# Kernel optimization log

Hardware: AMD Instinct MI355X
Metric: run time of the kernel (lower is better)

## Reference

```python
import jax, jax.numpy as jnp
import numpy as np

B, N, C = 1, 4096, 1024
H = 16
HD = C // H  # head_dim = 64
SCALE = HD ** -0.5


def setup_inputs() -> dict:
    key = jax.random.key(0)
    k1, k2, k3, k4, k5 = jax.random.split(key, 5)
    x1 = jax.random.normal(k1, (B, N, C), dtype=jnp.float32)
    x2 = jax.random.normal(k2, (B, N, C), dtype=jnp.float32)
    # qkv: Linear(dim, 2*all_head_dim), bias=False. Stored as (in, out) for x @ W.
    W_qkv = jax.random.normal(k3, (C, 2 * H * HD), dtype=jnp.float32) * (C ** -0.5)
    # proj: Linear(all_head_dim, dim) with bias
    W_proj = jax.random.normal(k4, (H * HD, C), dtype=jnp.float32) * ((H * HD) ** -0.5)
    b_proj = jax.random.normal(k5, (C,), dtype=jnp.float32) * 0.01
    return {"x1": x1, "x2": x2, "W_qkv": W_qkv, "W_proj": W_proj, "b_proj": b_proj}


def reference(x1, x2, W_qkv, W_proj, b_proj):
    b, n, c = x1.shape
    # qk projection: (B,N,2*H*HD) -> (2,B,H,N,HD)
    qkv = (x1 @ W_qkv).reshape(b, n, 2, H, HD).transpose(2, 0, 3, 1, 4)
    q, k = qkv[0], qkv[1]  # (B,H,N,HD)
    # V2: reshape (N,1,H,HD) then permute -> (1,H,N,HD); valid since B==1
    v = x2.reshape(n, 1, H, HD).transpose(1, 2, 0, 3)
    attn = jax.nn.softmax(jnp.einsum('bhnd,bhmd->bhnm', q * SCALE, k), axis=-1)
    out = jnp.einsum('bhnm,bhmd->bhnd', attn, v)  # broadcasts v over batch
    out = out.transpose(0, 2, 1, 3).reshape(b, n, H * HD)
    return out @ W_proj + b_proj
```

## Files before the change

kernel.cpp:

```cpp
#include <hip/hip_runtime.h>

typedef unsigned short u16;
typedef unsigned int u32;

#define HNUM 16
#define NSEQ 4096
#define CDIM 1024
#define SCALE 0.125f
#define LOG2E 1.4426950408889634f

using bf16x8 = __attribute__((ext_vector_type(8))) __bf16;
using f32x4  = __attribute__((ext_vector_type(4))) float;

__device__ __forceinline__ u16 f2bf(float f) {
  union { float f; u32 u; } v; v.f = f;
  u32 u = v.u;
  return (u16)((u + 0x7fffu + ((u >> 16) & 1u)) >> 16);
}
__device__ __forceinline__ float fexp2(float x) { return __builtin_amdgcn_exp2f(x); }

__device__ __forceinline__ f32x4 mfma16(bf16x8 a, bf16x8 b, f32x4 c) {
  return __builtin_amdgcn_mfma_f32_16x16x32_bf16(a, b, c, 0, 0, 0);
}

__device__ __forceinline__ u32 pack2(float a, float b) {
  union { float f; u32 u; } A, B;
  A.f = a; B.f = b;
  return __builtin_amdgcn_perm(B.u + 0x8000u, A.u + 0x8000u, 0x07060302u);
}

__device__ __forceinline__ void g2l16(const void* g, void* l) {
  __builtin_amdgcn_global_load_lds(
      (const __attribute__((address_space(1))) unsigned int*)(unsigned long long)g,
      (__attribute__((address_space(3))) unsigned int*)(unsigned int)(unsigned long long)l,
      16, 0, 0);
}

__global__ __launch_bounds__(256) void cvt_k(const float* __restrict__ in,
                                             u16* __restrict__ out) {
  const int i = (blockIdx.x * 256 + threadIdx.x) * 8;
  const float4 f0 = *(const float4*)(in + i);
  const float4 f1 = *(const float4*)(in + i + 4);
  u32 d[4] = {pack2(f0.x, f0.y), pack2(f0.z, f0.w),
              pack2(f1.x, f1.y), pack2(f1.z, f1.w)};
  *(bf16x8*)(out + i) = *(bf16x8*)d;
}

__global__ __launch_bounds__(256) void cvtT_k(const float* __restrict__ in,
                                              u16* __restrict__ out, int R, int C,
                                              int scaleRows, float scale) {
  __shared__ u16 t[64][65];
  const int tid = threadIdx.x;
  const int r0 = blockIdx.y * 64, c0 = blockIdx.x * 64;
  const int tr = tid >> 2, tc = (tid & 3) * 16;
  const float s = (c0 < scaleRows) ? scale : 1.0f;
  const float* src = in + (r0 + tr) * C + c0 + tc;
#pragma unroll
  for (int i = 0; i < 16; ++i) t[tr][tc + i] = f2bf(src[i] * s);
  __syncthreads();
  u16* dst = out + (c0 + tr) * R + r0 + tc;
#pragma unroll
  for (int i = 0; i < 16; ++i) dst[i] = t[tc + i][tr];
}

__global__ __launch_bounds__(256) void gemm1_k(const u16* __restrict__ A,
                                               const u16* __restrict__ Bt,
                                               u16* __restrict__ C,
                                               int M, int N, int K) {
  __shared__ __align__(16) u16 As[128 * 64];
  __shared__ __align__(16) u16 Bs[128 * 64];
  const int tid = threadIdx.x;
  const int wave = tid >> 6, lane = tid & 63;
  const int quad = lane >> 4, l16 = lane & 15;
  const int m0 = blockIdx.y * 128, n0 = blockIdx.x * 128;
  const int wm = (wave >> 1) * 64, wn = (wave & 1) * 64;
  const int lrow = lane >> 3, lc8 = (lane & 7) * 8;

  f32x4 acc[4][4] = {};
  for (int k0 = 0; k0 < K; k0 += 64) {
#pragma unroll
    for (int c = 0; c < 4; ++c) {
      const int cw = wave * 4 + c;
      g2l16(A  + (m0 + cw * 8 + lrow) * K + k0 + lc8, (char*)As + cw * 1024);
      g2l16(Bt + (n0 + cw * 8 + lrow) * K + k0 + lc8, (char*)Bs + cw * 1024);
    }
    __syncthreads();
#pragma unroll
    for (int ks = 0; ks < 2; ++ks) {
      bf16x8 a[4], b[4];
#pragma unroll
      for (int mt = 0; mt < 4; ++mt)
        a[mt] = *(const bf16x8*)(As + (wm + mt * 16 + l16) * 64 + ks * 32 + quad * 8);
#pragma unroll
      for (int nt = 0; nt < 4; ++nt)
        b[nt] = *(const bf16x8*)(Bs + (wn + nt * 16 + l16) * 64 + ks * 32 + quad * 8);
#pragma unroll
      for (int mt = 0; mt < 4; ++mt)
#pragma unroll
        for (int nt = 0; nt < 4; ++nt)
          acc[mt][nt] = mfma16(a[mt], b[nt], acc[mt][nt]);
    }
    __syncthreads();
  }
#pragma unroll
  for (int mt = 0; mt < 4; ++mt)
#pragma unroll
    for (int nt = 0; nt < 4; ++nt)
#pragma unroll
      for (int r = 0; r < 4; ++r)
        C[(m0 + wm + mt * 16 + quad * 4 + r) * N + n0 + wn + nt * 16 + l16] =
            f2bf(acc[mt][nt][r]);
}

__global__ __launch_bounds__(256) void gemm2_k(const u16* __restrict__ A,
                                               const u16* __restrict__ Bt,
                                               float* __restrict__ C,
                                               const float* __restrict__ bias,
                                               int M, int N, int K) {
  __shared__ __align__(16) u16 As[128 * 64];
  __shared__ __align__(16) u16 Bs[64 * 64];
  const int tid = threadIdx.x;
  const int wave = tid >> 6, lane = tid & 63;
  const int quad = lane >> 4, l16 = lane & 15;
  const int m0 = blockIdx.y * 128, n0 = blockIdx.x * 64;
  const int wm = wave * 32;
  const int lrow = lane >> 3, lc8 = (lane & 7) * 8;

  f32x4 acc[2][4] = {};
  for (int k0 = 0; k0 < K; k0 += 64) {
#pragma unroll
    for (int c = 0; c < 4; ++c) {
      const int cw = wave * 4 + c;
      g2l16(A + (m0 + cw * 8 + lrow) * K + k0 + lc8, (char*)As + cw * 1024);
    }
#pragma unroll
    for (int c = 0; c < 2; ++c) {
      const int cw = wave * 2 + c;
      g2l16(Bt + (n0 + cw * 8 + lrow) * K + k0 + lc8, (char*)Bs + cw * 1024);
    }
    __syncthreads();
#pragma unroll
    for (int ks = 0; ks < 2; ++ks) {
      bf16x8 a[2], b[4];
#pragma unroll
      for (int mt = 0; mt < 2; ++mt)
        a[mt] = *(const bf16x8*)(As + (wm + mt * 16 + l16) * 64 + ks * 32 + quad * 8);
#pragma unroll
      for (int nt = 0; nt < 4; ++nt)
        b[nt] = *(const bf16x8*)(Bs + (nt * 16 + l16) * 64 + ks * 32 + quad * 8);
#pragma unroll
      for (int mt = 0; mt < 2; ++mt)
#pragma unroll
        for (int nt = 0; nt < 4; ++nt)
          acc[mt][nt] = mfma16(a[mt], b[nt], acc[mt][nt]);
    }
    __syncthreads();
  }
#pragma unroll
  for (int mt = 0; mt < 2; ++mt)
#pragma unroll
    for (int nt = 0; nt < 4; ++nt)
#pragma unroll
      for (int r = 0; r < 4; ++r) {
        const int col = n0 + nt * 16 + l16;
        C[(m0 + wm + mt * 16 + quad * 4 + r) * N + col] = acc[mt][nt][r] + bias[col];
      }
}

__global__ __launch_bounds__(128) void attn_k(const u16* __restrict__ QK,
                                              const u16* __restrict__ Vt,
                                              u16* __restrict__ O) {
  __shared__ __align__(16) u16 Ks[2][64 * 64];
  __shared__ __align__(16) u16 Vs[2][64 * 64];
  __shared__ __align__(16) u16 Ps[2][32 * 64];
  const int tid = threadIdx.x;
  const int wave = tid >> 6, lane = tid & 63;
  const int quad = lane >> 4, l16 = lane & 15;
  const int head = blockIdx.y;
  const int qb = blockIdx.x * 64 + wave * 32;
  const int lrow = lane >> 3;
  const int lc8 = ((lane & 7) ^ lrow) * 8;
  const int swz = (quad ^ (l16 & 7)) * 8;

  const u16* kp[4];
  const u16* vp[4];
#pragma unroll
  for (int c = 0; c < 4; ++c) {
    const int row = (wave * 4 + c) * 8 + lrow;
    kp[c] = QK + row * 2048 + CDIM + head * 64 + lc8;
    vp[c] = Vt + (head * 64 + row) * NSEQ + lc8;
  }

  bf16x8 qf[2][2];
#pragma unroll
  for (int mt = 0; mt < 2; ++mt)
#pragma unroll
    for (int ks = 0; ks < 2; ++ks)
      qf[mt][ks] = *(const bf16x8*)(QK + (qb + mt * 16 + l16) * 2048 + head * 64 +
                                    ks * 32 + quad * 8);

  f32x4 o[2][4] = {};
  float lsum[2] = {};
  bf16x8 pfr[2][2];
  bf16x8 vfr[2][4];
  u16* Pw = Ps[wave];

#pragma unroll
  for (int c = 0; c < 4; ++c) {
    const int cw = wave * 4 + c;
    g2l16(kp[c], (char*)Ks[0] + cw * 1024);
    g2l16(vp[c], (char*)Vs[0] + cw * 1024);
    kp[c] += 64 * 2048;
    vp[c] += 64;
  }

  for (int kt = 0; kt < NSEQ / 64; ++kt) {
    const int cur = kt & 1;
    __syncthreads();

    if (kt > 0) {
#pragma unroll
      for (int ks = 0; ks < 2; ++ks)
#pragma unroll
        for (int dt = 0; dt < 4; ++dt)
#pragma unroll
          for (int mt = 0; mt < 2; ++mt)
            o[mt][dt] = mfma16(pfr[mt][ks], vfr[ks][dt], o[mt][dt]);
    }

    if (kt < NSEQ / 64 - 1) {
#pragma unroll
      for (int c = 0; c < 4; ++c) {
        const int cw = wave * 4 + c;
        g2l16(kp[c], (char*)Ks[1 - cur] + cw * 1024);
        g2l16(vp[c], (char*)Vs[1 - cur] + cw * 1024);
        kp[c] += 64 * 2048;
        vp[c] += 64;
      }
    }

    const u16* Kc = Ks[cur];
    const u16* Vc = Vs[cur];

    f32x4 s[2][4] = {};
#pragma unroll
    for (int ks = 0; ks < 2; ++ks)
#pragma unroll
      for (int nt = 0; nt < 4; ++nt) {
        const bf16x8 kf =
            *(const bf16x8*)(Kc + (nt * 16 + l16) * 64 + (swz ^ (ks * 32)));
#pragma unroll
        for (int mt = 0; mt < 2; ++mt)
          s[mt][nt] = mfma16(kf, qf[mt][ks], s[mt][nt]);
      }

#pragma unroll
    for (int mt = 0; mt < 2; ++mt)
#pragma unroll
      for (int nt = 0; nt < 4; ++nt) {
        const float p0 = fexp2(s[mt][nt][0]);
        const float p1 = fexp2(s[mt][nt][1]);
        const float p2 = fexp2(s[mt][nt][2]);
        const float p3 = fexp2(s[mt][nt][3]);
        lsum[mt] += (p0 + p1) + (p2 + p3);
        u32 d01 = pack2(p0, p1), d23 = pack2(p2, p3);
        const int col8 = (nt * 2 + (quad >> 1)) ^ (l16 & 7);
        u32* dst = (u32*)(Pw + (mt * 16 + l16) * 64 + col8 * 8 + (quad & 1) * 4);
        dst[0] = d01; dst[1] = d23;
      }

#pragma unroll
    for (int mt = 0; mt < 2; ++mt)
#pragma unroll
      for (int ks = 0; ks < 2; ++ks)
        pfr[mt][ks] = *(const bf16x8*)(Pw + (mt * 16 + l16) * 64 + (swz ^ (ks * 32)));
#pragma unroll
    for (int ks = 0; ks < 2; ++ks)
#pragma unroll
      for (int dt = 0; dt < 4; ++dt)
        vfr[ks][dt] =
            *(const bf16x8*)(Vc + (dt * 16 + l16) * 64 + (swz ^ (ks * 32)));
  }

#pragma unroll
  for (int ks = 0; ks < 2; ++ks)
#pragma unroll
    for (int dt = 0; dt < 4; ++dt)
#pragma unroll
      for (int mt = 0; mt < 2; ++mt)
        o[mt][dt] = mfma16(pfr[mt][ks], vfr[ks][dt], o[mt][dt]);

  float linv[2];
#pragma unroll
  for (int mt = 0; mt < 2; ++mt) {
    float v = lsum[mt];
    v += __shfl_xor(v, 16, 64);
    v += __shfl_xor(v, 32, 64);
    linv[mt] = 1.0f / v;
  }
#pragma unroll
  for (int mt = 0; mt < 2; ++mt)
#pragma unroll
    for (int r = 0; r < 4; ++r) {
      const float lv = __shfl(linv[mt], (lane & 48) | (quad * 4 + r), 64);
#pragma unroll
      for (int dt = 0; dt < 4; ++dt)
        O[(qb + mt * 16 + quad * 4 + r) * CDIM + head * 64 + dt * 16 + l16] =
            f2bf(o[mt][dt][r] * lv);
    }
}

extern "C" void kernel_launch(void* const* d_in, const int* in_sizes, int n_in,
                              void* d_out, int out_size, void* d_ws, size_t ws_size,
                              hipStream_t stream) {
  const float* x1    = (const float*)d_in[0];
  const float* x2    = (const float*)d_in[1];
  const float* Wqkv  = (const float*)d_in[2];
  const float* Wproj = (const float*)d_in[3];
  const float* bproj = (const float*)d_in[4];
  float* out = (float*)d_out;

  char* ws = (char*)d_ws;
  u16* QK  = (u16*)(ws);
  u16* Vt  = (u16*)(ws + 16u * 1024 * 1024);
  u16* Obf = (u16*)(ws + 24u * 1024 * 1024);
  u16* WpT = (u16*)(ws + 32u * 1024 * 1024);
  u16* WqT = (u16*)(ws + 34u * 1024 * 1024);
  u16* x1b = (u16*)(ws + 38u * 1024 * 1024);

  const float cfac = SCALE * LOG2E;

  cvt_k<<<dim3(4096 * 1024 / 2048), 256, 0, stream>>>(x1, x1b);
  cvtT_k<<<dim3(2048 / 64, 1024 / 64), 256, 0, stream>>>(Wqkv, WqT, 1024, 2048,
                                                         1024, cfac);
  cvtT_k<<<dim3(1024 / 64, 1024 / 64), 256, 0, stream>>>(Wproj, WpT, 1024, 1024,
                                                         0, 1.0f);
  cvtT_k<<<dim3(1024 / 64, 4096 / 64), 256, 0, stream>>>(x2, Vt, 4096, 1024,
                                                         0, 1.0f);

  gemm1_k<<<dim3(2048 / 128, 4096 / 128), 256, 0, stream>>>(x1b, WqT, QK,
                                                            4096, 2048, 1024);
  attn_k<<<dim3(4096 / 64, HNUM), 128, 0, stream>>>(QK, Vt, Obf);
  gemm2_k<<<dim3(1024 / 64, 4096 / 128), 256, 0, stream>>>(Obf, WpT, out, bproj,
                                                           4096, 1024, 1024);
}
```

Before: 249.6 us.

## Double-buffer GEMM LDS tiles and load attention K/V straight to registers

Both projection GEMMs gain a second LDS buffer. The next K-slice is prefetched while the current one feeds MFMAs, which removes one barrier per iteration. The attention kernel drops its shared K/V staging entirely: each wave loads K and V fragments from global memory into registers, prefetching the next K tile while the softmax runs, and keeps only the per-wave P buffer in LDS. This removes block-wide barriers and LDS traffic in attention, but each wave now fetches K/V separately with strided 16-byte loads, which relies on L2 and adds register pressure.

```diff
diff --git a/kernel.cpp b/kernel.cpp
--- a/kernel.cpp
+++ b/kernel.cpp
@@ -67,8 +67,8 @@
                                                const u16* __restrict__ Bt,
                                                u16* __restrict__ C,
                                                int M, int N, int K) {
-  __shared__ __align__(16) u16 As[128 * 64];
-  __shared__ __align__(16) u16 Bs[128 * 64];
+  __shared__ __align__(16) u16 As[2][128 * 64];
+  __shared__ __align__(16) u16 Bs[2][128 * 64];
   const int tid = threadIdx.x;
   const int wave = tid >> 6, lane = tid & 63;
   const int quad = lane >> 4, l16 = lane & 15;
@@ -77,30 +77,40 @@
   const int lrow = lane >> 3, lc8 = (lane & 7) * 8;
 
   f32x4 acc[4][4] = {};
-  for (int k0 = 0; k0 < K; k0 += 64) {
-#pragma unroll
-    for (int c = 0; c < 4; ++c) {
-      const int cw = wave * 4 + c;
-      g2l16(A  + (m0 + cw * 8 + lrow) * K + k0 + lc8, (char*)As + cw * 1024);
-      g2l16(Bt + (n0 + cw * 8 + lrow) * K + k0 + lc8, (char*)Bs + cw * 1024);
-    }
+#pragma unroll
+  for (int c = 0; c < 4; ++c) {
+    const int cw = wave * 4 + c;
+    g2l16(A  + (m0 + cw * 8 + lrow) * K + lc8, (char*)As[0] + cw * 1024);
+    g2l16(Bt + (n0 + cw * 8 + lrow) * K + lc8, (char*)Bs[0] + cw * 1024);
+  }
+  const int NIT = K / 64;
+  for (int it = 0; it < NIT; ++it) {
+    const int cur = it & 1;
     __syncthreads();
+    if (it + 1 < NIT) {
+      const int k0 = (it + 1) * 64;
+#pragma unroll
+      for (int c = 0; c < 4; ++c) {
+        const int cw = wave * 4 + c;
+        g2l16(A  + (m0 + cw * 8 + lrow) * K + k0 + lc8, (char*)As[1 - cur] + cw * 1024);
+        g2l16(Bt + (n0 + cw * 8 + lrow) * K + k0 + lc8, (char*)Bs[1 - cur] + cw * 1024);
+      }
+    }
 #pragma unroll
     for (int ks = 0; ks < 2; ++ks) {
       bf16x8 a[4], b[4];
 #pragma unroll
       for (int mt = 0; mt < 4; ++mt)
-        a[mt] = *(const bf16x8*)(As + (wm + mt * 16 + l16) * 64 + ks * 32 + quad * 8);
+        a[mt] = *(const bf16x8*)(As[cur] + (wm + mt * 16 + l16) * 64 + ks * 32 + quad * 8);
 #pragma unroll
       for (int nt = 0; nt < 4; ++nt)
-        b[nt] = *(const bf16x8*)(Bs + (wn + nt * 16 + l16) * 64 + ks * 32 + quad * 8);
+        b[nt] = *(const bf16x8*)(Bs[cur] + (wn + nt * 16 + l16) * 64 + ks * 32 + quad * 8);
 #pragma unroll
       for (int mt = 0; mt < 4; ++mt)
 #pragma unroll
         for (int nt = 0; nt < 4; ++nt)
           acc[mt][nt] = mfma16(a[mt], b[nt], acc[mt][nt]);
     }
-    __syncthreads();
   }
 #pragma unroll
   for (int mt = 0; mt < 4; ++mt)
@@ -117,8 +127,8 @@
                                                float* __restrict__ C,
                                                const float* __restrict__ bias,
                                                int M, int N, int K) {
-  __shared__ __align__(16) u16 As[128 * 64];
-  __shared__ __align__(16) u16 Bs[64 * 64];
+  __shared__ __align__(16) u16 As[2][128 * 64];
+  __shared__ __align__(16) u16 Bs[2][64 * 64];
   const int tid = threadIdx.x;
   const int wave = tid >> 6, lane = tid & 63;
   const int quad = lane >> 4, l16 = lane & 15;
@@ -127,34 +137,48 @@
   const int lrow = lane >> 3, lc8 = (lane & 7) * 8;
 
   f32x4 acc[2][4] = {};
-  for (int k0 = 0; k0 < K; k0 += 64) {
-#pragma unroll
-    for (int c = 0; c < 4; ++c) {
-      const int cw = wave * 4 + c;
-      g2l16(A + (m0 + cw * 8 + lrow) * K + k0 + lc8, (char*)As + cw * 1024);
-    }
-#pragma unroll
-    for (int c = 0; c < 2; ++c) {
-      const int cw = wave * 2 + c;
-      g2l16(Bt + (n0 + cw * 8 + lrow) * K + k0 + lc8, (char*)Bs + cw * 1024);
-    }
+#pragma unroll
+  for (int c = 0; c < 4; ++c) {
+    const int cw = wave * 4 + c;
+    g2l16(A + (m0 + cw * 8 + lrow) * K + lc8, (char*)As[0] + cw * 1024);
+  }
+#pragma unroll
+  for (int c = 0; c < 2; ++c) {
+    const int cw = wave * 2 + c;
+    g2l16(Bt + (n0 + cw * 8 + lrow) * K + lc8, (char*)Bs[0] + cw * 1024);
+  }
+  const int NIT = K / 64;
+  for (int it = 0; it < NIT; ++it) {
+    const int cur = it & 1;
     __syncthreads();
+    if (it + 1 < NIT) {
+      const int k0 = (it + 1) * 64;
+#pragma unroll
+      for (int c = 0; c < 4; ++c) {
+        const int cw = wave * 4 + c;
+        g2l16(A + (m0 + cw * 8 + lrow) * K + k0 + lc8, (char*)As[1 - cur] + cw * 1024);
+      }
+#pragma unroll
+      for (int c = 0; c < 2; ++c) {
+        const int cw = wave * 2 + c;
+        g2l16(Bt + (n0 + cw * 8 + lrow) * K + k0 + lc8, (char*)Bs[1 - cur] + cw * 1024);
+      }
+    }
 #pragma unroll
     for (int ks = 0; ks < 2; ++ks) {
       bf16x8 a[2], b[4];
 #pragma unroll
       for (int mt = 0; mt < 2; ++mt)
-        a[mt] = *(const bf16x8*)(As + (wm + mt * 16 + l16) * 64 + ks * 32 + quad * 8);
+        a[mt] = *(const bf16x8*)(As[cur] + (wm + mt * 16 + l16) * 64 + ks * 32 + quad * 8);
 #pragma unroll
       for (int nt = 0; nt < 4; ++nt)
-        b[nt] = *(const bf16x8*)(Bs + (nt * 16 + l16) * 64 + ks * 32 + quad * 8);
+        b[nt] = *(const bf16x8*)(Bs[cur] + (nt * 16 + l16) * 64 + ks * 32 + quad * 8);
 #pragma unroll
       for (int mt = 0; mt < 2; ++mt)
 #pragma unroll
         for (int nt = 0; nt < 4; ++nt)
           acc[mt][nt] = mfma16(a[mt], b[nt], acc[mt][nt]);
     }
-    __syncthreads();
   }
 #pragma unroll
   for (int mt = 0; mt < 2; ++mt)
@@ -170,26 +194,16 @@
 __global__ __launch_bounds__(128) void attn_k(const u16* __restrict__ QK,
                                               const u16* __restrict__ Vt,
                                               u16* __restrict__ O) {
-  __shared__ __align__(16) u16 Ks[2][64 * 64];
-  __shared__ __align__(16) u16 Vs[2][64 * 64];
   __shared__ __align__(16) u16 Ps[2][32 * 64];
   const int tid = threadIdx.x;
   const int wave = tid >> 6, lane = tid & 63;
   const int quad = lane >> 4, l16 = lane & 15;
   const int head = blockIdx.y;
   const int qb = blockIdx.x * 64 + wave * 32;
-  const int lrow = lane >> 3;
-  const int lc8 = ((lane & 7) ^ lrow) * 8;
   const int swz = (quad ^ (l16 & 7)) * 8;
 
-  const u16* kp[4];
-  const u16* vp[4];
-#pragma unroll
-  for (int c = 0; c < 4; ++c) {
-    const int row = (wave * 4 + c) * 8 + lrow;
-    kp[c] = QK + row * 2048 + CDIM + head * 64 + lc8;
-    vp[c] = Vt + (head * 64 + row) * NSEQ + lc8;
-  }
+  const u16* kbase = QK + l16 * 2048 + CDIM + head * 64 + quad * 8;
+  const u16* vbase = Vt + (head * 64 + l16) * 4096 + quad * 8;
 
   bf16x8 qf[2][2];
 #pragma unroll
@@ -201,58 +215,40 @@
 
   f32x4 o[2][4] = {};
   float lsum[2] = {};
-  bf16x8 pfr[2][2];
-  bf16x8 vfr[2][4];
   u16* Pw = Ps[wave];
 
-#pragma unroll
-  for (int c = 0; c < 4; ++c) {
-    const int cw = wave * 4 + c;
-    g2l16(kp[c], (char*)Ks[0] + cw * 1024);
-    g2l16(vp[c], (char*)Vs[0] + cw * 1024);
-    kp[c] += 64 * 2048;
-    vp[c] += 64;
-  }
-
-  for (int kt = 0; kt < NSEQ / 64; ++kt) {
-    const int cur = kt & 1;
-    __syncthreads();
-
-    if (kt > 0) {
+  bf16x8 kf[2][4];
+#pragma unroll
+  for (int ks = 0; ks < 2; ++ks)
+#pragma unroll
+    for (int nt = 0; nt < 4; ++nt)
+      kf[ks][nt] = *(const bf16x8*)(kbase + (nt * 16) * 2048 + ks * 32);
+
+  for (int kt0 = 0; kt0 < NSEQ; kt0 += 64) {
+    bf16x8 vf[2][4];
+#pragma unroll
+    for (int ks = 0; ks < 2; ++ks)
+#pragma unroll
+      for (int dt = 0; dt < 4; ++dt)
+        vf[ks][dt] = *(const bf16x8*)(vbase + (dt * 16) * 4096 + kt0 + ks * 32);
+
+    f32x4 s[2][4] = {};
+#pragma unroll
+    for (int ks = 0; ks < 2; ++ks)
+#pragma unroll
+      for (int nt = 0; nt < 4; ++nt)
+#pragma unroll
+        for (int mt = 0; mt < 2; ++mt)
+          s[mt][nt] = mfma16(kf[ks][nt], qf[mt][ks], s[mt][nt]);
+
+    if (kt0 + 64 < NSEQ) {
 #pragma unroll
       for (int ks = 0; ks < 2; ++ks)
 #pragma unroll
-        for (int dt = 0; dt < 4; ++dt)
-#pragma unroll
-          for (int mt = 0; mt < 2; ++mt)
-            o[mt][dt] = mfma16(pfr[mt][ks], vfr[ks][dt], o[mt][dt]);
-    }
-
-    if (kt < NSEQ / 64 - 1) {
-#pragma unroll
-      for (int c = 0; c < 4; ++c) {
-        const int cw = wave * 4 + c;
-        g2l16(kp[c], (char*)Ks[1 - cur] + cw * 1024);
-        g2l16(vp[c], (char*)Vs[1 - cur] + cw * 1024);
-        kp[c] += 64 * 2048;
-        vp[c] += 64;
-      }
-    }
-
-    const u16* Kc = Ks[cur];
-    const u16* Vc = Vs[cur];
-
-    f32x4 s[2][4] = {};
-#pragma unroll
-    for (int ks = 0; ks < 2; ++ks)
-#pragma unroll
-      for (int nt = 0; nt < 4; ++nt) {
-        const bf16x8 kf =
-            *(const bf16x8*)(Kc + (nt * 16 + l16) * 64 + (swz ^ (ks * 32)));
-#pragma unroll
-        for (int mt = 0; mt < 2; ++mt)
-          s[mt][nt] = mfma16(kf, qf[mt][ks], s[mt][nt]);
-      }
+        for (int nt = 0; nt < 4; ++nt)
+          kf[ks][nt] =
+              *(const bf16x8*)(kbase + (kt0 + 64 + nt * 16) * 2048 + ks * 32);
+    }
 
 #pragma unroll
     for (int mt = 0; mt < 2; ++mt)
@@ -270,25 +266,18 @@
       }
 
 #pragma unroll
-    for (int mt = 0; mt < 2; ++mt)
-#pragma unroll
-      for (int ks = 0; ks < 2; ++ks)
-        pfr[mt][ks] = *(const bf16x8*)(Pw + (mt * 16 + l16) * 64 + (swz ^ (ks * 32)));
-#pragma unroll
-    for (int ks = 0; ks < 2; ++ks)
+    for (int ks = 0; ks < 2; ++ks) {
+      bf16x8 pf[2];
+#pragma unroll
+      for (int mt = 0; mt < 2; ++mt)
+        pf[mt] = *(const bf16x8*)(Pw + (mt * 16 + l16) * 64 + (swz ^ (ks * 32)));
 #pragma unroll
       for (int dt = 0; dt < 4; ++dt)
-        vfr[ks][dt] =
-            *(const bf16x8*)(Vc + (dt * 16 + l16) * 64 + (swz ^ (ks * 32)));
-  }
-
-#pragma unroll
-  for (int ks = 0; ks < 2; ++ks)
-#pragma unroll
-    for (int dt = 0; dt < 4; ++dt)
-#pragma unroll
-      for (int mt = 0; mt < 2; ++mt)
-        o[mt][dt] = mfma16(pfr[mt][ks], vfr[ks][dt], o[mt][dt]);
+#pragma unroll
+        for (int mt = 0; mt < 2; ++mt)
+          o[mt][dt] = mfma16(pf[mt], vf[ks][dt], o[mt][dt]);
+    }
+  }
 
   float linv[2];
 #pragma unroll
```

After: 367.5 us. 47.2% more time.
